# Kernel tuning notes

Measured on AMD Instinct MI355X. Metric: run time of the kernel, lower is better.

Reference implementation:

```python
import jax, jax.numpy as jnp
import numpy as np

NUM_HEADS = 16
HEAD_DIM = 64
MIN_FREQ = 1.0
MAX_FREQ = 40.0


def _rope_cos_sin(t, dtype):
    # golden_gate RoPE, pos_dim=1: geometric frequency ladder in [min_freq, max_freq],
    # positions normalized to [0,1) so max_freq ~ highest spatial frequency.
    n = HEAD_DIM // 2
    j = jnp.arange(n, dtype=dtype)
    freqs = MIN_FREQ * (MAX_FREQ / MIN_FREQ) ** (j / (n - 1))  # [n]
    pos = jnp.arange(t, dtype=dtype) / t                        # [t]
    theta = 2.0 * jnp.pi * pos[:, None] * freqs[None, :]        # [t, n]
    return jnp.cos(theta), jnp.sin(theta)


def _apply_rope(x, cos, sin):
    # x: [b, h, t, d]; rotate-half convention
    n = HEAD_DIM // 2
    x1, x2 = x[..., :n], x[..., n:]
    return jnp.concatenate([x1 * cos - x2 * sin, x1 * sin + x2 * cos], axis=-1)


def setup_inputs() -> dict:
    key = jax.random.key(0)
    ks = jax.random.split(key, 5)
    b, t, c = 4, 2048, 1024
    s = 1.0 / np.sqrt(c)
    return {
        "x": jax.random.normal(ks[0], (b, t, c), dtype=jnp.float32),
        "qkv_w": jax.random.normal(ks[1], (3 * c, c), dtype=jnp.float32) * s,
        "qkv_b": jax.random.normal(ks[2], (3 * c,), dtype=jnp.float32) * 0.01,
        "proj_w": jax.random.normal(ks[3], (c, c), dtype=jnp.float32) * s,
        "proj_b": jax.random.normal(ks[4], (c,), dtype=jnp.float32) * 0.01,
    }


def reference(x, qkv_w, qkv_b, proj_w, proj_b):
    b, t, c = x.shape
    h, d = NUM_HEADS, HEAD_DIM
    qkv = x @ qkv_w.T + qkv_b                                   # [b, t, 3c]
    qkv = qkv.reshape(b, t, 3, h, d).transpose(0, 3, 1, 2, 4)   # [b, h, t, 3, d]
    q, k, v = qkv[..., 0, :], qkv[..., 1, :], qkv[..., 2, :]    # each [b, h, t, d]
    cos, sin = _rope_cos_sin(t, x.dtype)
    q = _apply_rope(q, cos, sin)
    k = _apply_rope(k, cos, sin)
    scale = 1.0 / jnp.sqrt(jnp.asarray(d, dtype=x.dtype))
    scores = jnp.einsum("bhqd,bhkd->bhqk", q, k) * scale        # [b, h, t, t]
    attn = jax.nn.softmax(scores, axis=-1)
    out = jnp.einsum("bhqk,bhkd->bhqd", attn, v)                # [b, h, t, d]
    out = out.transpose(0, 2, 1, 3).reshape(b, t, h * d)        # [b, t, c]
    return out @ proj_w.T + proj_b
```

## Files before the change

kernel.cpp:

```cpp
#include <hip/hip_runtime.h>

typedef unsigned short u16;
typedef unsigned int   u32;
typedef __attribute__((ext_vector_type(8))) short s16x8;
typedef __attribute__((ext_vector_type(4))) float f32x4;
typedef __attribute__((ext_vector_type(16))) float f32x16;

#define MFMA16(a, b, c) __builtin_amdgcn_mfma_f32_16x16x32_bf16((a), (b), (c), 0, 0, 0)
#define MFMA32(a, b, c) __builtin_amdgcn_mfma_f32_32x32x16_bf16((a), (b), (c), 0, 0, 0)
#define EXP2R(x) __builtin_amdgcn_exp2f(x)

#define GLD16(gp, lp) __builtin_amdgcn_global_load_lds(                     \
    (const __attribute__((address_space(1))) void*)(gp),                    \
    (__attribute__((address_space(3))) void*)(lp), 16, 0, 0)

#define PWOFF 1048576ull

__device__ __forceinline__ u16 f2b(float f) {
  union { float f; unsigned i; } x; x.f = f;
  unsigned r = x.i + 0x7FFFu + ((x.i >> 16) & 1u);
  return (u16)(r >> 16);
}
__device__ __forceinline__ u32 cvtpk_bf16(float a, float b) {
  u32 r;
  asm("v_cvt_pk_bf16_f32 %0, %1, %2" : "=v"(r) : "v"(a), "v"(b));
  return r;
}
__device__ __forceinline__ s16x8 cvt8(const float* __restrict__ p) {
  f32x4 a = *(const f32x4*)p;
  f32x4 b = *(const f32x4*)(p + 4);
  union { u32 u[4]; s16x8 v; } o;
  o.u[0] = cvtpk_bf16(a[0], a[1]);
  o.u[1] = cvtpk_bf16(a[2], a[3]);
  o.u[2] = cvtpk_bf16(b[0], b[1]);
  o.u[3] = cvtpk_bf16(b[2], b[3]);
  return o.v;
}

__device__ __forceinline__ void plswap(u32& a, u32& b) {
#if __has_builtin(__builtin_amdgcn_permlane32_swap)
  auto r = __builtin_amdgcn_permlane32_swap(a, b, false, false);
  a = r[0]; b = r[1];
#else
  asm volatile("v_permlane32_swap_b32 %0, %1" : "+v"(a), "+v"(b));
#endif
}
__device__ __forceinline__ float pair32(float x, int hi) {
  union { float f; u32 u; } a, b;
  a.f = x; b.f = x;
  plswap(a.u, b.u);
  return hi ? a.f : b.f;
}
__device__ __forceinline__ s16x8 mk_pa(float e0, float e1, float e2, float e3,
                                       float e4, float e5, float e6, float e7) {
  u32 a0 = cvtpk_bf16(e0, e1), b0 = cvtpk_bf16(e4, e5);
  u32 a1 = cvtpk_bf16(e2, e3), b1 = cvtpk_bf16(e6, e7);
  plswap(a0, b0);
  plswap(a1, b1);
  union { u32 u[4]; s16x8 v; } x;
  x.u[0] = a0; x.u[1] = a1; x.u[2] = b0; x.u[3] = b1;
  return x.v;
}

#define SM_GRP(sv, ofs, pa_out, ps_out) {                                  \
    float e0 = EXP2R((sv)[(ofs) + 0] * C - mC);                            \
    float e1 = EXP2R((sv)[(ofs) + 1] * C - mC);                            \
    float e2 = EXP2R((sv)[(ofs) + 2] * C - mC);                            \
    float e3 = EXP2R((sv)[(ofs) + 3] * C - mC);                            \
    float e4 = EXP2R((sv)[(ofs) + 4] * C - mC);                            \
    float e5 = EXP2R((sv)[(ofs) + 5] * C - mC);                            \
    float e6 = EXP2R((sv)[(ofs) + 6] * C - mC);                            \
    float e7 = EXP2R((sv)[(ofs) + 7] * C - mC);                            \
    (pa_out) = mk_pa(e0, e1, e2, e3, e4, e5, e6, e7);                      \
    (ps_out) = ((e0 + e1) + (e2 + e3)) + ((e4 + e5) + (e6 + e7));          \
  }

__global__ void k_beacon(float* __restrict__ Out, unsigned long long ws_size) {
  float V = 3000.0f + fminf((float)(ws_size >> 20), 999.0f);
  size_t i = ((size_t)blockIdx.x * 256 + threadIdx.x) * 8;
#pragma unroll
  for (int j = 0; j < 8; ++j) Out[i + j] = V;
}

__global__ void k_convert_pw(const float* __restrict__ PW, u16* __restrict__ ws) {
  size_t i = ((size_t)blockIdx.x * 256 + threadIdx.x) * 8;
  *(s16x8*)(ws + i) = cvt8(PW + i);
}

__global__ void k_convert_xw(const float* __restrict__ X,
                             const float* __restrict__ W,
                             u16* __restrict__ dst) {
  size_t i = ((size_t)blockIdx.x * 256 + threadIdx.x) * 8;
  const float* src = (i < 8388608ull) ? (X + i) : (W + (i - 8388608ull));
  *(s16x8*)(dst + i) = cvt8(src);
}

#define QLOAD(K) {                                                 \
    la0 = *(const f32x4*)(Ag + (K));                               \
    la1 = *(const f32x4*)(Ag + (K) + 4);                           \
    lb0 = *(const f32x4*)(Ag + (size_t)64 * 1024 + (K));           \
    lb1 = *(const f32x4*)(Ag + (size_t)64 * 1024 + (K) + 4);       \
    lc0 = *(const f32x4*)(BgA + (K));                              \
    lc1 = *(const f32x4*)(BgA + (K) + 4);                          \
    ld0 = *(const f32x4*)(BgB + (K));                              \
    ld1 = *(const f32x4*)(BgB + (K) + 4);                          \
  }
#define QWRITE(BUF) {                                                         \
    union { u32 u[4]; s16x8 v; } t0, t1, t2, t3;                              \
    t0.u[0] = cvtpk_bf16(la0[0], la0[1]); t0.u[1] = cvtpk_bf16(la0[2], la0[3]); \
    t0.u[2] = cvtpk_bf16(la1[0], la1[1]); t0.u[3] = cvtpk_bf16(la1[2], la1[3]); \
    t1.u[0] = cvtpk_bf16(lb0[0], lb0[1]); t1.u[1] = cvtpk_bf16(lb0[2], lb0[3]); \
    t1.u[2] = cvtpk_bf16(lb1[0], lb1[1]); t1.u[3] = cvtpk_bf16(lb1[2], lb1[3]); \
    t2.u[0] = cvtpk_bf16(lc0[0], lc0[1]); t2.u[1] = cvtpk_bf16(lc0[2], lc0[3]); \
    t2.u[2] = cvtpk_bf16(lc1[0], lc1[1]); t2.u[3] = cvtpk_bf16(lc1[2], lc1[3]); \
    t3.u[0] = cvtpk_bf16(ld0[0], ld0[1]); t3.u[1] = cvtpk_bf16(ld0[2], ld0[3]); \
    t3.u[2] = cvtpk_bf16(ld1[0], ld1[1]); t3.u[3] = cvtpk_bf16(ld1[2], ld1[3]); \
    *(s16x8*)&(BUF)[srow * 32 + scol]               = t0.v;                   \
    *(s16x8*)&(BUF)[(srow + 64) * 32 + scol]        = t1.v;                   \
    *(s16x8*)&(BUF)[4096 + srow * 32 + scol]        = t2.v;                   \
    *(s16x8*)&(BUF)[4096 + (srow + 64) * 32 + scol] = t3.v;                   \
  }

#define QISSUEB(K, BUF) {                                          \
    GLD16(Agb + (K),          (BUF) + w * 512);                    \
    GLD16(Agb + 65536 + (K),  (BUF) + 2048 + w * 512);             \
    GLD16(BgAb + (K),         (BUF) + 4096 + w * 512);             \
    GLD16(BgBb + (K),         (BUF) + 6144 + w * 512);             \
  }

#define QKV_EPILOGUE                                                          \
  const int ncol = n0 + wc * 64;                   \
  const int which = ncol >> lgHB;                            \
  const int hh = (ncol & (HB - 1)) >> 6;                                      \
  const int cb = which * 1024 + (h0 + hh) * 64;                               \
  const int mbase = m0 + wr * 64;                                             \
  float bias[4];                                                              \
  _Pragma("unroll")                                                           \
  for (int j = 0; j < 4; ++j) bias[j] = Bias[cb + j * 16 + l16];              \
  __syncthreads();                                                            \
  u16* OSt = smem + w * 4608;                                                 \
  if (which == 2) {                                                           \
    _Pragma("unroll")                                                         \
    for (int i = 0; i < 4; ++i)                                               \
      _Pragma("unroll")                                                       \
      for (int r = 0; r < 4; ++r) {                                           \
        int tl = i * 16 + quad * 4 + r;                                       \
        _Pragma("unroll")                                                     \
        for (int j = 0; j < 4; ++j)                                           \
          OSt[(j * 16 + l16) * 72 + tl] = f2b(acc[i][j][r] + bias[j]);        \
      }                                                                       \
  } else {                                                                    \
    const float LC = 0.1716750968f;                                           \
    float fr0 = exp2f((float)l16 * LC);                                       \
    float fr1 = exp2f((float)(16 + l16) * LC);                                \
    _Pragma("unroll")                                                         \
    for (int i = 0; i < 4; ++i)                                               \
      _Pragma("unroll")                                                       \
      for (int r = 0; r < 4; ++r) {                                           \
        int tl = i * 16 + quad * 4 + r;                                       \
        int tok = mbase + tl;                                                 \
        float ps = (float)(tok & 2047) * (1.0f / 2048.0f);                    \
        float rv0 = ps * fr0; rv0 -= floorf(rv0);                             \
        float rv1 = ps * fr1; rv1 -= floorf(rv1);                             \
        float s0 = __builtin_amdgcn_sinf(rv0), c0 = __builtin_amdgcn_cosf(rv0); \
        float s1 = __builtin_amdgcn_sinf(rv1), c1 = __builtin_amdgcn_cosf(rv1); \
        float x10 = acc[i][0][r] + bias[0], x11 = acc[i][1][r] + bias[1];     \
        float x20 = acc[i][2][r] + bias[2], x21 = acc[i][3][r] + bias[3];     \
        OSt[tl * 72 + l16]      = f2b(x10 * c0 - x20 * s0);                   \
        OSt[tl * 72 + 16 + l16] = f2b(x11 * c1 - x21 * s1);                   \
        OSt[tl * 72 + 32 + l16] = f2b(x10 * s0 + x20 * c0);                   \
        OSt[tl * 72 + 48 + l16] = f2b(x11 * s1 + x21 * c1);                   \
      }                                                                       \
  }                                                                           \
  const int bb = mbase >> 11, tt0 = mbase & 2047;                             \
  const int pp = (bb << lgHG) + hh;                                           \
  if (which == 2) {                                                           \
    u16* D = Vc + ((size_t)pp * 32 + (tt0 >> 6)) * 4096;                      \
    _Pragma("unroll")                                                         \
    for (int fi = 0; fi < 8; ++fi) {                                          \
      int ks = fi >> 1, db = fi & 1;                                          \
      *(s16x8*)&D[fi * 512 + lane * 8] =                                      \
          *(const s16x8*)&OSt[(db * 32 + l31) * 72 + ks * 16 + hi * 8];       \
    }                                                                         \
  } else if (which == 1) {                                                    \
    u16* D = Kc + ((size_t)pp * 32 + (tt0 >> 6)) * 4096;                      \
    _Pragma("unroll")                                                         \
    for (int fi = 0; fi < 8; ++fi) {                                          \
      int ks = fi >> 1, kb = fi & 1;                                          \
      *(s16x8*)&D[fi * 512 + lane * 8] =                                      \
          *(const s16x8*)&OSt[(kb * 32 + l31) * 72 + ks * 16 + hi * 8];       \
    }                                                                         \
  } else {                                                                    \
    u16* D = Qc + ((size_t)pp * 64 + (tt0 >> 5)) * 2048;                      \
    _Pragma("unroll")                                                         \
    for (int fi = 0; fi < 8; ++fi) {                                          \
      int qh = fi >> 2, ks = fi & 3;                                          \
      *(s16x8*)&D[(size_t)qh * 2048 + ks * 512 + lane * 8] =                  \
          *(const s16x8*)&OSt[(qh * 32 + l31) * 72 + ks * 16 + hi * 8];       \
    }                                                                         \
  }

__global__ __launch_bounds__(256, 4) void k_qkv_rope(
    const float* __restrict__ X, const float* __restrict__ W,
    const float* __restrict__ Bias, u16* __restrict__ ws,
    int h0, int lgHB, int lgHG)
{
  __shared__ __align__(16) u16 smem[18432];

  const size_t segE = 524288ull << lgHG;
  u16* Qc = ws + PWOFF;
  u16* Kc = Qc + segE;
  u16* Vc = Kc + segE;

  const int tid = threadIdx.x;
  const int w = tid >> 6, lane = tid & 63, quad = lane >> 4, l16 = lane & 15;
  const int l31 = lane & 31, hi = lane >> 5;
  const int wr = w >> 1, wc = w & 1;
  const int HB = 1 << lgHB;

  const int gx = gridDim.x;
  const int hw = blockIdx.y * gx + blockIdx.x;
  const int cpx = (gx << 6) >> 3;
  const int lg = (hw & 7) * cpx + (hw >> 3);
  const int m0 = (lg / gx) * 128, n0 = (lg % gx) * 128;

  const f32x4 z4 = {0.f, 0.f, 0.f, 0.f};
  f32x4 acc[4][4];
#pragma unroll
  for (int i = 0; i < 4; ++i)
#pragma unroll
    for (int j = 0; j < 4; ++j) acc[i][j] = z4;

  const int srow = tid >> 2;
  const int scol = (tid & 3) * 8;
  const int nlogA = n0 + srow, nlogB = nlogA + 64;
  const int wrowA = (nlogA >> lgHB) * 1024 + (h0 + ((nlogA & (HB - 1)) >> 6)) * 64 + (nlogA & 63);
  const int wrowB = (nlogB >> lgHB) * 1024 + (h0 + ((nlogB & (HB - 1)) >> 6)) * 64 + (nlogB & 63);
  const float* Ag  = X + (size_t)(m0 + srow) * 1024 + scol;
  const float* BgA = W + (size_t)wrowA * 1024 + scol;
  const float* BgB = W + (size_t)wrowB * 1024 + scol;

  f32x4 la0, la1, lb0, lb1, lc0, lc1, ld0, ld1;
  QLOAD(0)
  QWRITE(smem)

  for (int k0 = 0; k0 < 1024; k0 += 32) {
    u16* Ac = smem + ((k0 >> 5) & 1) * 8192;
    if (k0 < 992) QLOAD(k0 + 32)
    __syncthreads();
    s16x8 af[4], bf[4];
#pragma unroll
    for (int i = 0; i < 4; ++i)
      af[i] = *(const s16x8*)&Ac[(wr * 64 + i * 16 + l16) * 32 + quad * 8];
#pragma unroll
    for (int j = 0; j < 4; ++j)
      bf[j] = *(const s16x8*)&Ac[4096 + (wc * 64 + j * 16 + l16) * 32 + quad * 8];
#pragma unroll
    for (int i = 0; i < 4; ++i)
#pragma unroll
      for (int j = 0; j < 4; ++j)
        acc[i][j] = MFMA16(af[i], bf[j], acc[i][j]);
    if (k0 < 992) {
      u16* An = smem + ((~(k0 >> 5)) & 1) * 8192;
      QWRITE(An)
    }
  }

  QKV_EPILOGUE
}

__global__ __launch_bounds__(256, 4) void k_qkv_rope_b(
    const u16* __restrict__ Xb, const u16* __restrict__ Wb,
    const float* __restrict__ Bias, u16* __restrict__ ws,
    int h0, int lgHB, int lgHG)
{
  __shared__ __align__(16) u16 smem[18432];

  const size_t segE = 524288ull << lgHG;
  u16* Qc = ws + PWOFF;
  u16* Kc = Qc + segE;
  u16* Vc = Kc + segE;

  const int tid = threadIdx.x;
  const int w = tid >> 6, lane = tid & 63, quad = lane >> 4, l16 = lane & 15;
  const int l31 = lane & 31, hi = lane >> 5;
  const int wr = w >> 1, wc = w & 1;
  const int HB = 1 << lgHB;

  const int gx = gridDim.x;
  const int hw = blockIdx.y * gx + blockIdx.x;
  const int cpx = (gx << 6) >> 3;
  const int lg = (hw & 7) * cpx + (hw >> 3);
  const int m0 = (lg / gx) * 128, n0 = (lg % gx) * 128;

  const f32x4 z4 = {0.f, 0.f, 0.f, 0.f};
  f32x4 acc[4][4];
#pragma unroll
  for (int i = 0; i < 4; ++i)
#pragma unroll
    for (int j = 0; j < 4; ++j) acc[i][j] = z4;

  const int srow = tid >> 2;
  const int scol = (tid & 3) * 8;
  const int nlogA = n0 + srow, nlogB = nlogA + 64;
  const int wrowA = (nlogA >> lgHB) * 1024 + (h0 + ((nlogA & (HB - 1)) >> 6)) * 64 + (nlogA & 63);
  const int wrowB = (nlogB >> lgHB) * 1024 + (h0 + ((nlogB & (HB - 1)) >> 6)) * 64 + (nlogB & 63);
  const u16* Agb  = Xb + (size_t)(m0 + srow) * 1024 + scol;
  const u16* BgAb = Wb + (size_t)wrowA * 1024 + scol;
  const u16* BgBb = Wb + (size_t)wrowB * 1024 + scol;

  QISSUEB(0, smem)

  for (int k0 = 0; k0 < 1024; k0 += 32) {
    u16* Ac = smem + ((k0 >> 5) & 1) * 8192;
    __syncthreads();
    if (k0 < 992) {
      u16* An = smem + ((~(k0 >> 5)) & 1) * 8192;
      QISSUEB(k0 + 32, An)
    }
    s16x8 af[4], bf[4];
#pragma unroll
    for (int i = 0; i < 4; ++i)
      af[i] = *(const s16x8*)&Ac[(wr * 64 + i * 16 + l16) * 32 + quad * 8];
#pragma unroll
    for (int j = 0; j < 4; ++j)
      bf[j] = *(const s16x8*)&Ac[4096 + (wc * 64 + j * 16 + l16) * 32 + quad * 8];
#pragma unroll
    for (int i = 0; i < 4; ++i)
#pragma unroll
      for (int j = 0; j < 4; ++j)
        acc[i][j] = MFMA16(af[i], bf[j], acc[i][j]);
  }

  QKV_EPILOGUE
}

__global__ __launch_bounds__(256, 4) void k_attn(
    u16* __restrict__ ws, u16* __restrict__ AO, int h0, int lgHG)
{
  __shared__ float redL[4][32];

  const size_t segE = 524288ull << lgHG;
  const u16* Qg = ws + PWOFF;
  const u16* Kg = Qg + segE;
  const u16* Vg = Kg + segE;

  const int tid = threadIdx.x;
  const int w = tid >> 6, lane = tid & 63;
  const int l31 = lane & 31, hi = lane >> 5;

  const int P = 4 << lgHG;
  const int n = blockIdx.y * 16 + blockIdx.x;
  const int mm = n >> 3;
  const int p  = (n & 7) * (P >> 3) + (mm >> 4);
  const int qt = mm & 15;

  const u16* Kb = Kg + (size_t)p * 131072;
  const u16* Vb = Vg + (size_t)p * 131072;
  const int q0 = qt * 128 + w * 32;

  const u16* Qt = Qg + (size_t)p * 131072 + (size_t)(qt * 4 + w) * 2048;
  s16x8 qf[4];
#pragma unroll
  for (int ks = 0; ks < 4; ++ks)
    qf[ks] = *(const s16x8*)&Qt[ks * 512 + lane * 8];

  f32x16 o0, o1;
#pragma unroll
  for (int r = 0; r < 16; ++r) { o0[r] = 0.f; o1[r] = 0.f; }
  float m_r = -1e30f, li = 0.f;
  const float C = 0.1803368801f;

  for (int kt = 0; kt < 32; ++kt) {
    const u16* Kt = Kb + (size_t)kt * 4096;
    const u16* Vt = Vb + (size_t)kt * 4096;
    s16x8 kfA[4], kfB[4], vfA[4], vfB[4];
#pragma unroll
    for (int ks = 0; ks < 4; ++ks) {
      kfA[ks] = *(const s16x8*)&Kt[(ks * 2 + 0) * 512 + lane * 8];
      kfB[ks] = *(const s16x8*)&Kt[(ks * 2 + 1) * 512 + lane * 8];
    }
#pragma unroll
    for (int ks = 0; ks < 4; ++ks) {
      vfA[ks] = *(const s16x8*)&Vt[(ks * 2 + 0) * 512 + lane * 8];
      vfB[ks] = *(const s16x8*)&Vt[(ks * 2 + 1) * 512 + lane * 8];
    }

    f32x16 s0, s1;
#pragma unroll
    for (int r = 0; r < 16; ++r) { s0[r] = 0.f; s1[r] = 0.f; }
#pragma unroll
    for (int ks = 0; ks < 4; ++ks) {
      s0 = MFMA32(kfA[ks], qf[ks], s0);
      s1 = MFMA32(kfB[ks], qf[ks], s1);
    }

    float m8[8];
#pragma unroll
    for (int r = 0; r < 8; ++r)
      m8[r] = fmaxf(fmaxf(s0[r], s0[r + 8]), fmaxf(s1[r], s1[r + 8]));
    float mx = fmaxf(fmaxf(fmaxf(m8[0], m8[1]), fmaxf(m8[2], m8[3])),
                     fmaxf(fmaxf(m8[4], m8[5]), fmaxf(m8[6], m8[7])));
    mx = fmaxf(mx, pair32(mx, hi));

    if (!__all(mx - m_r <= 8.0f)) {
      float mnew = fmaxf(m_r, mx);
      float al = EXP2R((m_r - mnew) * C);
      m_r = mnew;
      li *= al;
      if (hi == 0) redL[w][l31] = al;
      f32x4 a0 = *(const f32x4*)&redL[w][hi * 4];
      f32x4 a1 = *(const f32x4*)&redL[w][8 + hi * 4];
      f32x4 a2 = *(const f32x4*)&redL[w][16 + hi * 4];
      f32x4 a3 = *(const f32x4*)&redL[w][24 + hi * 4];
#pragma unroll
      for (int e = 0; e < 4; ++e) {
        o0[e]      *= a0[e];  o1[e]      *= a0[e];
        o0[4 + e]  *= a1[e];  o1[4 + e]  *= a1[e];
        o0[8 + e]  *= a2[e];  o1[8 + e]  *= a2[e];
        o0[12 + e] *= a3[e];  o1[12 + e] *= a3[e];
      }
    }

    const float mC = m_r * C;
    s16x8 pa0, pa1, pa2, pa3;
    float ps0, ps1, ps2, ps3;
    SM_GRP(s0, 0, pa0, ps0);
    SM_GRP(s0, 8, pa1, ps1);
    SM_GRP(s1, 0, pa2, ps2);
    SM_GRP(s1, 8, pa3, ps3);
    float sum = (ps0 + ps1) + (ps2 + ps3);
    sum += pair32(sum, hi);
    li += sum;

    o0 = MFMA32(pa0, vfA[0], o0);  o1 = MFMA32(pa0, vfB[0], o1);
    o0 = MFMA32(pa1, vfA[1], o0);  o1 = MFMA32(pa1, vfB[1], o1);
    o0 = MFMA32(pa2, vfA[2], o0);  o1 = MFMA32(pa2, vfB[2], o1);
    o0 = MFMA32(pa3, vfA[3], o0);  o1 = MFMA32(pa3, vfB[3], o1);
  }

  if (hi == 0) redL[w][l31] = 1.0f / li;
  f32x4 i0 = *(const f32x4*)&redL[w][hi * 4];
  f32x4 i1 = *(const f32x4*)&redL[w][8 + hi * 4];
  f32x4 i2 = *(const f32x4*)&redL[w][16 + hi * 4];
  f32x4 i3 = *(const f32x4*)&redL[w][24 + hi * 4];

  const int p_glob = (p >> lgHG) * 16 + h0 + (p & ((1 << lgHG) - 1));
  u16* Ab = AO + (size_t)p_glob * 131072 + (size_t)q0 * 64;
#pragma unroll
  for (int g = 0; g < 4; ++g) {
    const f32x4 iv = (g == 0) ? i0 : (g == 1) ? i1 : (g == 2) ? i2 : i3;
#pragma unroll
    for (int e = 0; e < 4; ++e) {
      int row = g * 8 + hi * 4 + e;
      Ab[(size_t)row * 64 + l31]      = f2b(o0[g * 4 + e] * iv[e]);
      Ab[(size_t)row * 64 + 32 + l31] = f2b(o1[g * 4 + e] * iv[e]);
    }
  }
}

#define PISSUE(K, BUF) {                                                     \
    const int c0_ = (K) + scol;                                              \
    GLD16(Abase + (size_t)(c0_ >> 6) * 131072 + (c0_ & 63), (BUF) + w * 512); \
    GLD16(Bg + (K),          (BUF) + 2048 + w * 512);                        \
    GLD16(Bg + 65536 + (K),  (BUF) + 4096 + w * 512);                        \
  }

__global__ __launch_bounds__(256, 4) void k_proj(
    const u16* __restrict__ AO, const u16* __restrict__ W,
    const float* __restrict__ Bias, float* __restrict__ Out)
{
  __shared__ __align__(16) u16 smem[12288];

  const int tid = threadIdx.x;
  const int w = tid >> 6, lane = tid & 63, quad = lane >> 4, l16 = lane & 15;

  const int hw = blockIdx.y * 8 + blockIdx.x;
  const int lg = (hw & 7) * 128 + (hw >> 3);
  const int m0 = (lg >> 3) * 64, n0 = (lg & 7) * 128;

  const f32x4 z4 = {0.f, 0.f, 0.f, 0.f};
  f32x4 acc[4][2];
#pragma unroll
  for (int i = 0; i < 4; ++i)
#pragma unroll
    for (int j = 0; j < 2; ++j) acc[i][j] = z4;

  const int srow = tid >> 2;
  const int scol = (tid & 3) * 8;
  const int bb = m0 >> 11, tt = m0 & 2047;
  const u16* Abase = AO + (size_t)bb * 2097152 + (size_t)(tt + srow) * 64;
  const u16* Bg = W + (size_t)(n0 + srow) * 1024 + scol;

  PISSUE(0, smem)

  for (int k0 = 0; k0 < 1024; k0 += 32) {
    u16* Ac = smem + ((k0 >> 5) & 1) * 6144;
    __syncthreads();
    if (k0 < 992) {
      u16* An = smem + ((~(k0 >> 5)) & 1) * 6144;
      PISSUE(k0 + 32, An)
    }
    s16x8 af[4], bf[2];
#pragma unroll
    for (int i = 0; i < 4; ++i)
      af[i] = *(const s16x8*)&Ac[(i * 16 + l16) * 32 + quad * 8];
#pragma unroll
    for (int j = 0; j < 2; ++j)
      bf[j] = *(const s16x8*)&Ac[2048 + (w * 32 + j * 16 + l16) * 32 + quad * 8];
#pragma unroll
    for (int i = 0; i < 4; ++i)
#pragma unroll
      for (int j = 0; j < 2; ++j)
        acc[i][j] = MFMA16(af[i], bf[j], acc[i][j]);
  }

  const int ncol = n0 + w * 32;
  float bias[2];
#pragma unroll
  for (int j = 0; j < 2; ++j) bias[j] = Bias[ncol + j * 16 + l16];

  __syncthreads();
  float* OSw = (float*)smem + w * 512;
#pragma unroll
  for (int i = 0; i < 4; ++i) {
#pragma unroll
    for (int j = 0; j < 2; ++j)
#pragma unroll
      for (int r = 0; r < 4; ++r)
        OSw[(quad * 4 + r) * 32 + j * 16 + l16] = acc[i][j][r] + bias[j];
#pragma unroll
    for (int itr = 0; itr < 2; ++itr) {
      int task = itr * 64 + lane;
      int tl = task >> 3, g = task & 7;
      *(f32x4*)&Out[(size_t)(m0 + i * 16 + tl) * 1024 + ncol + g * 4] =
          *(const f32x4*)&OSw[tl * 32 + g * 4];
    }
  }
}

extern "C" void kernel_launch(void* const* d_in, const int* in_sizes, int n_in,
                              void* d_out, int out_size, void* d_ws, size_t ws_size,
                              hipStream_t stream) {
  const float* X    = (const float*)d_in[0];
  const float* QKVW = (const float*)d_in[1];
  const float* QKVB = (const float*)d_in[2];
  const float* PW   = (const float*)d_in[3];
  const float* PB   = (const float*)d_in[4];
  float* Out = (float*)d_out;
  u16* ws = (u16*)d_ws;

  int HG, lgHG, ok = 1;
  if      (ws_size >= 52428800ull) { HG = 16; lgHG = 4; }
  else if (ws_size >= 44040192ull) { HG = 8;  lgHG = 3; }
  else if (ws_size >= 31457280ull) { HG = 4;  lgHG = 2; }
  else if (ws_size >= 25165824ull) { HG = 2;  lgHG = 1; }
  else                             { HG = 2;  lgHG = 1; ok = 0; }

  if (!ok) {
    k_beacon<<<dim3(4096), 256, 0, stream>>>(Out, (unsigned long long)ws_size);
    return;
  }

  const size_t segE = 524288ull << lgHG;
  u16* Qc = ws + PWOFF;
  u16* AO = (HG == 16) ? Qc : (Qc + 3 * segE);
  const int lgHB = lgHG + 6;

  const bool fast = (HG == 16) && (ws_size >= 75497472ull);
  u16* Xb = Qc + 3 * segE;
  u16* Wb = Xb + 8388608ull;

  k_convert_pw<<<dim3(512), 256, 0, stream>>>(PW, ws);
  if (fast)
    k_convert_xw<<<dim3(5632), 256, 0, stream>>>(X, QKVW, Xb);

  const int chunks = 16 / HG;
  for (int c = 0; c < chunks; ++c) {
    int h0 = c * HG;
    if (fast)
      k_qkv_rope_b<<<dim3((3 * HG) / 2, 64), 256, 0, stream>>>(
          Xb, Wb, QKVB, ws, h0, lgHB, lgHG);
    else
      k_qkv_rope<<<dim3((3 * HG) / 2, 64), 256, 0, stream>>>(
          X, QKVW, QKVB, ws, h0, lgHB, lgHG);
    k_attn<<<dim3(16, 4 * HG), 256, 0, stream>>>(ws, AO, h0, lgHG);
  }
  k_proj<<<dim3(8, 128), 256, 0, stream>>>(AO, ws, PB, Out);
}
```

Baseline: 306.7 us.

## Process two query tiles per wave in attention to reuse K/V fragments

Each attention wave now handles two 32-row query tiles (A and B) against the same K/V fragments loaded per key tile, halving the grid in x and halving K/V global loads per query row. The per-tile math is factored into macros and run twice per iteration, which gives independent MFMA/softmax chains that can interleave. Register pressure roughly doubles for accumulators, so launch bounds drop from 4 to 2 waves per EU, lowering occupancy.

```diff
diff --git a/kernel.cpp b/kernel.cpp
--- a/kernel.cpp
+++ b/kernel.cpp
@@ -73,6 +73,84 @@
     float e7 = EXP2R((sv)[(ofs) + 7] * C - mC);                            \
     (pa_out) = mk_pa(e0, e1, e2, e3, e4, e5, e6, e7);                      \
     (ps_out) = ((e0 + e1) + (e2 + e3)) + ((e4 + e5) + (e6 + e7));          \
+  }
+
+#define QKT_P(QF, KA, KB, S0, S1) {                                        \
+    _Pragma("unroll")                                                      \
+    for (int r = 0; r < 16; ++r) { (S0)[r] = 0.f; (S1)[r] = 0.f; }         \
+    _Pragma("unroll")                                                      \
+    for (int ks = 0; ks < 4; ++ks) {                                       \
+      (S0) = MFMA32((KA)[ks], (QF)[ks], (S0));                             \
+      (S1) = MFMA32((KB)[ks], (QF)[ks], (S1));                             \
+    }                                                                      \
+  }
+
+#define SMAX_P(S0, S1, PA0, PA1, PA2, PA3, MR, LI, O0, O1) {               \
+    float m8[8];                                                           \
+    _Pragma("unroll")                                                      \
+    for (int r = 0; r < 8; ++r)                                            \
+      m8[r] = fmaxf(fmaxf((S0)[r], (S0)[r + 8]),                           \
+                    fmaxf((S1)[r], (S1)[r + 8]));                          \
+    float mx = fmaxf(fmaxf(fmaxf(m8[0], m8[1]), fmaxf(m8[2], m8[3])),      \
+                     fmaxf(fmaxf(m8[4], m8[5]), fmaxf(m8[6], m8[7])));     \
+    mx = fmaxf(mx, pair32(mx, hi));                                        \
+    if (!__all(mx - (MR) <= 8.0f)) {                                       \
+      float mnew = fmaxf((MR), mx);                                        \
+      float al = EXP2R(((MR) - mnew) * C);                                 \
+      (MR) = mnew;                                                         \
+      (LI) *= al;                                                          \
+      if (hi == 0) redL[w][l31] = al;                                      \
+      f32x4 a0 = *(const f32x4*)&redL[w][hi * 4];                          \
+      f32x4 a1 = *(const f32x4*)&redL[w][8 + hi * 4];                      \
+      f32x4 a2 = *(const f32x4*)&redL[w][16 + hi * 4];                     \
+      f32x4 a3 = *(const f32x4*)&redL[w][24 + hi * 4];                     \
+      _Pragma("unroll")                                                    \
+      for (int e = 0; e < 4; ++e) {                                        \
+        (O0)[e]      *= a0[e];  (O1)[e]      *= a0[e];                     \
+        (O0)[4 + e]  *= a1[e];  (O1)[4 + e]  *= a1[e];                     \
+        (O0)[8 + e]  *= a2[e];  (O1)[8 + e]  *= a2[e];                     \
+        (O0)[12 + e] *= a3[e];  (O1)[12 + e] *= a3[e];                     \
+      }                                                                    \
+    }                                                                      \
+    const float mC = (MR) * C;                                             \
+    float ps0, ps1, ps2, ps3;                                              \
+    SM_GRP(S0, 0, PA0, ps0);                                               \
+    SM_GRP(S0, 8, PA1, ps1);                                               \
+    SM_GRP(S1, 0, PA2, ps2);                                               \
+    SM_GRP(S1, 8, PA3, ps3);                                               \
+    float sum = (ps0 + ps1) + (ps2 + ps3);                                 \
+    sum += pair32(sum, hi);                                                \
+    (LI) += sum;                                                           \
+  }
+
+#define PV_P(PA0, PA1, PA2, PA3, VA, VB, O0, O1) {                         \
+    (O0) = MFMA32((PA0), (VA)[0], (O0));                                   \
+    (O1) = MFMA32((PA0), (VB)[0], (O1));                                   \
+    (O0) = MFMA32((PA1), (VA)[1], (O0));                                   \
+    (O1) = MFMA32((PA1), (VB)[1], (O1));                                   \
+    (O0) = MFMA32((PA2), (VA)[2], (O0));                                   \
+    (O1) = MFMA32((PA2), (VB)[2], (O1));                                   \
+    (O0) = MFMA32((PA3), (VA)[3], (O0));                                   \
+    (O1) = MFMA32((PA3), (VB)[3], (O1));                                   \
+  }
+
+#define ATT_EPI(LI, O0, O1, Q0) {                                          \
+    if (hi == 0) redL[w][l31] = 1.0f / (LI);                               \
+    f32x4 i0 = *(const f32x4*)&redL[w][hi * 4];                            \
+    f32x4 i1 = *(const f32x4*)&redL[w][8 + hi * 4];                        \
+    f32x4 i2 = *(const f32x4*)&redL[w][16 + hi * 4];                       \
+    f32x4 i3 = *(const f32x4*)&redL[w][24 + hi * 4];                       \
+    u16* Ab = AO + (size_t)p_glob * 131072 + (size_t)(Q0) * 64;            \
+    _Pragma("unroll")                                                      \
+    for (int g = 0; g < 4; ++g) {                                          \
+      const f32x4 iv = (g == 0) ? i0 : (g == 1) ? i1 : (g == 2) ? i2 : i3; \
+      _Pragma("unroll")                                                    \
+      for (int e = 0; e < 4; ++e) {                                        \
+        int row = g * 8 + hi * 4 + e;           \
+        Ab[(size_t)row * 64 + l31]      = f2b((O0)[g * 4 + e] * iv[e]);    \
+        Ab[(size_t)row * 64 + 32 + l31] = f2b((O1)[g * 4 + e] * iv[e]);    \
+      }                                                                    \
+    }                                                                      \
   }
 
 __global__ void k_beacon(float* __restrict__ Out, unsigned long long ws_size) {
@@ -335,7 +413,7 @@
   QKV_EPILOGUE
 }
 
-__global__ __launch_bounds__(256, 4) void k_attn(
+__global__ __launch_bounds__(256, 2) void k_attn(
     u16* __restrict__ ws, u16* __restrict__ AO, int h0, int lgHG)
 {
   __shared__ float redL[4][32];
@@ -350,25 +428,29 @@
   const int l31 = lane & 31, hi = lane >> 5;
 
   const int P = 4 << lgHG;
-  const int n = blockIdx.y * 16 + blockIdx.x;
+  const int n = blockIdx.y * 8 + blockIdx.x;
   const int mm = n >> 3;
-  const int p  = (n & 7) * (P >> 3) + (mm >> 4);
-  const int qt = mm & 15;
+  const int p  = (n & 7) * (P >> 3) + (mm >> 3);
+  const int qt = mm & 7;
 
   const u16* Kb = Kg + (size_t)p * 131072;
   const u16* Vb = Vg + (size_t)p * 131072;
-  const int q0 = qt * 128 + w * 32;
-
-  const u16* Qt = Qg + (size_t)p * 131072 + (size_t)(qt * 4 + w) * 2048;
-  s16x8 qf[4];
-#pragma unroll
-  for (int ks = 0; ks < 4; ++ks)
-    qf[ks] = *(const s16x8*)&Qt[ks * 512 + lane * 8];
-
-  f32x16 o0, o1;
-#pragma unroll
-  for (int r = 0; r < 16; ++r) { o0[r] = 0.f; o1[r] = 0.f; }
-  float m_r = -1e30f, li = 0.f;
+  const int q0A = qt * 256 + w * 32;
+  const int q0B = q0A + 128;
+
+  const u16* QtA = Qg + (size_t)p * 131072 + (size_t)(qt * 8 + w) * 2048;
+  const u16* QtB = QtA + 4 * 2048;
+  s16x8 qfA[4], qfB[4];
+#pragma unroll
+  for (int ks = 0; ks < 4; ++ks) {
+    qfA[ks] = *(const s16x8*)&QtA[ks * 512 + lane * 8];
+    qfB[ks] = *(const s16x8*)&QtB[ks * 512 + lane * 8];
+  }
+
+  f32x16 oA0, oA1, oB0, oB1;
+#pragma unroll
+  for (int r = 0; r < 16; ++r) { oA0[r] = 0.f; oA1[r] = 0.f; oB0[r] = 0.f; oB1[r] = 0.f; }
+  float mA = -1e30f, lA = 0.f, mB = -1e30f, lB = 0.f;
   const float C = 0.1803368801f;
 
   for (int kt = 0; kt < 32; ++kt) {
@@ -386,77 +468,25 @@
       vfB[ks] = *(const s16x8*)&Vt[(ks * 2 + 1) * 512 + lane * 8];
     }
 
-    f32x16 s0, s1;
-#pragma unroll
-    for (int r = 0; r < 16; ++r) { s0[r] = 0.f; s1[r] = 0.f; }
-#pragma unroll
-    for (int ks = 0; ks < 4; ++ks) {
-      s0 = MFMA32(kfA[ks], qf[ks], s0);
-      s1 = MFMA32(kfB[ks], qf[ks], s1);
-    }
-
-    float m8[8];
-#pragma unroll
-    for (int r = 0; r < 8; ++r)
-      m8[r] = fmaxf(fmaxf(s0[r], s0[r + 8]), fmaxf(s1[r], s1[r + 8]));
-    float mx = fmaxf(fmaxf(fmaxf(m8[0], m8[1]), fmaxf(m8[2], m8[3])),
-                     fmaxf(fmaxf(m8[4], m8[5]), fmaxf(m8[6], m8[7])));
-    mx = fmaxf(mx, pair32(mx, hi));
-
-    if (!__all(mx - m_r <= 8.0f)) {
-      float mnew = fmaxf(m_r, mx);
-      float al = EXP2R((m_r - mnew) * C);
-      m_r = mnew;
-      li *= al;
-      if (hi == 0) redL[w][l31] = al;
-      f32x4 a0 = *(const f32x4*)&redL[w][hi * 4];
-      f32x4 a1 = *(const f32x4*)&redL[w][8 + hi * 4];
-      f32x4 a2 = *(const f32x4*)&redL[w][16 + hi * 4];
-      f32x4 a3 = *(const f32x4*)&redL[w][24 + hi * 4];
-#pragma unroll
-      for (int e = 0; e < 4; ++e) {
-        o0[e]      *= a0[e];  o1[e]      *= a0[e];
-        o0[4 + e]  *= a1[e];  o1[4 + e]  *= a1[e];
-        o0[8 + e]  *= a2[e];  o1[8 + e]  *= a2[e];
-        o0[12 + e] *= a3[e];  o1[12 + e] *= a3[e];
-      }
-    }
-
-    const float mC = m_r * C;
-    s16x8 pa0, pa1, pa2, pa3;
-    float ps0, ps1, ps2, ps3;
-    SM_GRP(s0, 0, pa0, ps0);
-    SM_GRP(s0, 8, pa1, ps1);
-    SM_GRP(s1, 0, pa2, ps2);
-    SM_GRP(s1, 8, pa3, ps3);
-    float sum = (ps0 + ps1) + (ps2 + ps3);
-    sum += pair32(sum, hi);
-    li += sum;
-
-    o0 = MFMA32(pa0, vfA[0], o0);  o1 = MFMA32(pa0, vfB[0], o1);
-    o0 = MFMA32(pa1, vfA[1], o0);  o1 = MFMA32(pa1, vfB[1], o1);
-    o0 = MFMA32(pa2, vfA[2], o0);  o1 = MFMA32(pa2, vfB[2], o1);
-    o0 = MFMA32(pa3, vfA[3], o0);  o1 = MFMA32(pa3, vfB[3], o1);
-  }
-
-  if (hi == 0) redL[w][l31] = 1.0f / li;
-  f32x4 i0 = *(const f32x4*)&redL[w][hi * 4];
-  f32x4 i1 = *(const f32x4*)&redL[w][8 + hi * 4];
-  f32x4 i2 = *(const f32x4*)&redL[w][16 + hi * 4];
-  f32x4 i3 = *(const f32x4*)&redL[w][24 + hi * 4];
+    f32x16 sA0, sA1, sB0, sB1;
+    QKT_P(qfA, kfA, kfB, sA0, sA1)
+    QKT_P(qfB, kfA, kfB, sB0, sB1)
+
+    {
+      s16x8 pa0, pa1, pa2, pa3;
+      SMAX_P(sA0, sA1, pa0, pa1, pa2, pa3, mA, lA, oA0, oA1)
+      PV_P(pa0, pa1, pa2, pa3, vfA, vfB, oA0, oA1)
+    }
+    {
+      s16x8 pa0, pa1, pa2, pa3;
+      SMAX_P(sB0, sB1, pa0, pa1, pa2, pa3, mB, lB, oB0, oB1)
+      PV_P(pa0, pa1, pa2, pa3, vfA, vfB, oB0, oB1)
+    }
+  }
 
   const int p_glob = (p >> lgHG) * 16 + h0 + (p & ((1 << lgHG) - 1));
-  u16* Ab = AO + (size_t)p_glob * 131072 + (size_t)q0 * 64;
-#pragma unroll
-  for (int g = 0; g < 4; ++g) {
-    const f32x4 iv = (g == 0) ? i0 : (g == 1) ? i1 : (g == 2) ? i2 : i3;
-#pragma unroll
-    for (int e = 0; e < 4; ++e) {
-      int row = g * 8 + hi * 4 + e;
-      Ab[(size_t)row * 64 + l31]      = f2b(o0[g * 4 + e] * iv[e]);
-      Ab[(size_t)row * 64 + 32 + l31] = f2b(o1[g * 4 + e] * iv[e]);
-    }
-  }
+  ATT_EPI(lA, oA0, oA1, q0A)
+  ATT_EPI(lB, oB0, oB1, q0B)
 }
 
 #define PISSUE(K, BUF) {                                                     \
@@ -584,7 +614,7 @@
     else
       k_qkv_rope<<<dim3((3 * HG) / 2, 64), 256, 0, stream>>>(
           X, QKVW, QKVB, ws, h0, lgHB, lgHG);
-    k_attn<<<dim3(16, 4 * HG), 256, 0, stream>>>(ws, AO, h0, lgHG);
+    k_attn<<<dim3(8, 4 * HG), 256, 0, stream>>>(ws, AO, h0, lgHG);
   }
   k_proj<<<dim3(8, 128), 256, 0, stream>>>(AO, ws, PB, Out);
 }
```

Measured after the change: 277.4 us. 1.11x faster.
